# Kernel tuning notes

Hardware: AMD Instinct MI355X
Metric: run time of the kernel (lower is better)

The kernel has to match this reference:

```python
import jax, jax.numpy as jnp
import numpy as np

N = 50000   # nodes
E = 600000  # edges
D = 128     # in = hidden = out channels (must be equal per the cat/mean readout)
B = 4096    # number of lookup indices


def setup_inputs() -> dict:
    key = jax.random.key(0)
    ks = jax.random.split(key, 8)
    x = jax.random.normal(ks[0], (N, D), dtype=jnp.float32)
    edge_index = jax.random.randint(ks[1], (2, E), 0, N)
    edge_weight = jax.random.uniform(ks[2], (E,), dtype=jnp.float32)
    inputs_idx = jax.random.randint(ks[3], (B,), 0, N + 1)  # N is the appended zero row
    def lin_w(k, din, dout):
        return jax.random.normal(k, (din, dout), dtype=jnp.float32) / np.sqrt(din).astype(np.float32)
    W1 = lin_w(ks[4], D, D); b1 = jnp.zeros((D,), jnp.float32)
    W2 = lin_w(ks[5], D, D); b2 = jnp.zeros((D,), jnp.float32)
    W3 = lin_w(ks[6], D, D); b3 = jnp.zeros((D,), jnp.float32)
    return {"inputs_idx": inputs_idx, "x": x, "edge_index": edge_index,
            "edge_weight": edge_weight, "W1": W1, "b1": b1, "W2": W2,
            "b2": b2, "W3": W3, "b3": b3}


def gcn_conv(x, W, b, src, dst, w):
    # PyG GCNConv with add_self_loops=True (fill weight 1) and symmetric norm.
    deg = jnp.zeros((N,), x.dtype).at[dst].add(w) + 1.0  # self-loop contributes 1
    dinv = jax.lax.rsqrt(deg)
    norm = dinv[src] * w * dinv[dst]                      # [E]
    h = x @ W                                             # [N, D]
    agg = jax.ops.segment_sum(norm[:, None] * h[src], dst, num_segments=N)
    agg = agg + h * (dinv * dinv)[:, None]                # self-loop term: deg^-1 * h
    return agg + b


def lookup(x, inputs_idx):
    # append a zero row, then gather
    x_ = jnp.concatenate([x, jnp.zeros((1, x.shape[-1]), x.dtype)], axis=0)
    return x_[inputs_idx]  # [B, D]


def reference(inputs_idx, x, edge_index, edge_weight, W1, b1, W2, b2, W3, b3):
    src, dst = edge_index[0], edge_index[1]
    x1 = jax.nn.relu(gcn_conv(x, W1, b1, src, dst, edge_weight))
    x2 = jax.nn.relu(gcn_conv(x1, W2, b2, src, dst, edge_weight))
    x3 = jax.nn.relu(gcn_conv(x2, W3, b3, src, dst, edge_weight))
    e1 = lookup(x1, inputs_idx)
    e2 = lookup(x2, inputs_idx)
    e3 = lookup(x3, inputs_idx)
    # torch.cat([1,B,D]x3, dim=0).mean(0) == elementwise mean of the three
    return (e1 + e2 + e3) / 3.0
```

## Files before the change

### kernel.cpp

```cpp
#include <hip/hip_runtime.h>
#include <hip/hip_fp16.h>

#define D 128
#define STRIDE 48

typedef _Float16 f16x8 __attribute__((ext_vector_type(8)));
typedef float f32x4 __attribute__((ext_vector_type(4)));
struct h4 { __half2 a, b; };

__global__ __launch_bounds__(256) void zero_kernel(int* __restrict__ p, int n) {
  int i = blockIdx.x * 256 + threadIdx.x;
  if (i < n) p[i] = 0;
}

__global__ __launch_bounds__(256) void build_kernel(
    const int* __restrict__ ei, const float* __restrict__ ew,
    int* __restrict__ cnt, int2* __restrict__ pairs, int E) {
  int e = blockIdx.x * 256 + threadIdx.x;
  if (e >= E) return;
  int s = ei[e], d = ei[E + e];
  int rank = atomicAdd(&cnt[d], 1);
  if (rank < STRIDE) pairs[(size_t)d * STRIDE + rank] = make_int2(s, __float_as_int(ew[e]));
}

__global__ __launch_bounds__(256) void deg_dinv_kernel(
    int* __restrict__ cnt, const int2* __restrict__ pairs,
    float* __restrict__ dinv, int N) {
  int n = blockIdx.x * 4 + (threadIdx.x >> 6);
  int lane = threadIdx.x & 63;
  if (n >= N) return;
  int c = cnt[n];
  c = c < STRIDE ? c : STRIDE;
  float v = (lane < c) ? __int_as_float(pairs[(size_t)n * STRIDE + lane].y) : 0.f;
#pragma unroll
  for (int o = 32; o > 0; o >>= 1) v += __shfl_xor(v, o, 64);
  if (lane == 0) {
    dinv[n] = rsqrtf(v + 1.0f);
    cnt[n] = c;
  }
}

__global__ __launch_bounds__(256) void norm_kernel(
    const int* __restrict__ cnt, const float* __restrict__ dinv,
    int2* __restrict__ pairs, int N) {
  int n = blockIdx.x * 4 + (threadIdx.x >> 6);
  int lane = threadIdx.x & 63;
  if (n >= N) return;
  int c = cnt[n];
  float di = dinv[n];
  if (lane < c) {
    int2 p = pairs[(size_t)n * STRIDE + lane];
    p.y = __float_as_int(dinv[p.x] * __int_as_float(p.y) * di);
    pairs[(size_t)n * STRIDE + lane] = p;
  }
}

__global__ __launch_bounds__(256) void tohalf_kernel(
    const float* __restrict__ in, __half* __restrict__ out, int n4) {
  int t = blockIdx.x * 256 + threadIdx.x;
  if (t >= n4) return;
  float4 v = ((const float4*)in)[t];
  h4 o = {__floats2half2_rn(v.x, v.y), __floats2half2_rn(v.z, v.w)};
  ((h4*)out)[t] = o;
}

__global__ __launch_bounds__(256) void wtrans_kernel(
    const float* __restrict__ W1, const float* __restrict__ W2,
    const float* __restrict__ W3, __half* __restrict__ WT1,
    __half* __restrict__ WT2, __half* __restrict__ WT3) {
  int t = blockIdx.x * 256 + threadIdx.x;
  if (t >= 3 * D * D) return;
  int m = t >> 14;
  int i = t & (D * D - 1);
  int k = i >> 7, n = i & 127;
  const float* W = (m == 0) ? W1 : (m == 1) ? W2 : W3;
  __half* WT = (m == 0) ? WT1 : (m == 1) ? WT2 : WT3;
  WT[n * D + k] = __float2half(W[k * D + n]);
}

__global__ __launch_bounds__(256) void agg_kernel(
    const __half* __restrict__ x16, const float* __restrict__ dinv,
    const int* __restrict__ cnt, const int2* __restrict__ pairs,
    __half* __restrict__ agg16, int N) {
  int gw = (blockIdx.x * 256 + threadIdx.x) >> 6;
  int lane = threadIdx.x & 63;
  if (gw >= N) return;
  const __half2* xs = (const __half2*)x16;
  float di = dinv[gw];
  int c = cnt[gw];
  const int2* pr = pairs + (size_t)gw * STRIDE;
  float2 acc = __half22float2(xs[(size_t)gw * 64 + lane]);
  acc.x *= di * di;
  acc.y *= di * di;
  int e = 0;
  for (; e + 4 <= c; e += 4) {
    int2 p0 = pr[e], p1 = pr[e + 1], p2 = pr[e + 2], p3 = pr[e + 3];
    float n0 = __int_as_float(p0.y), n1 = __int_as_float(p1.y);
    float n2 = __int_as_float(p2.y), n3 = __int_as_float(p3.y);
    float2 v0 = __half22float2(xs[(size_t)p0.x * 64 + lane]);
    float2 v1 = __half22float2(xs[(size_t)p1.x * 64 + lane]);
    float2 v2 = __half22float2(xs[(size_t)p2.x * 64 + lane]);
    float2 v3 = __half22float2(xs[(size_t)p3.x * 64 + lane]);
    acc.x += n0 * v0.x + n1 * v1.x + n2 * v2.x + n3 * v3.x;
    acc.y += n0 * v0.y + n1 * v1.y + n2 * v2.y + n3 * v3.y;
  }
  for (; e < c; e++) {
    int2 p0 = pr[e];
    float n0 = __int_as_float(p0.y);
    float2 v0 = __half22float2(xs[(size_t)p0.x * 64 + lane]);
    acc.x += n0 * v0.x;
    acc.y += n0 * v0.y;
  }
  ((__half2*)agg16)[(size_t)gw * 64 + lane] = __floats2half2_rn(acc.x, acc.y);
}

__global__ __launch_bounds__(256) void agg_idx_kernel(
    const __half* __restrict__ x16, const float* __restrict__ dinv,
    const int* __restrict__ cnt, const int2* __restrict__ pairs,
    const int* __restrict__ idx, __half* __restrict__ aggI, int B, int N) {
  int gw = (blockIdx.x * 256 + threadIdx.x) >> 6;
  int lane = threadIdx.x & 63;
  if (gw >= B) return;
  const __half2* xs = (const __half2*)x16;
  float2 acc = make_float2(0.f, 0.f);
  int node = idx[gw];
  if ((unsigned)node < (unsigned)N) {
    float di = dinv[node];
    int c = cnt[node];
    const int2* pr = pairs + (size_t)node * STRIDE;
    acc = __half22float2(xs[(size_t)node * 64 + lane]);
    acc.x *= di * di;
    acc.y *= di * di;
    int e = 0;
    for (; e + 4 <= c; e += 4) {
      int2 p0 = pr[e], p1 = pr[e + 1], p2 = pr[e + 2], p3 = pr[e + 3];
      float n0 = __int_as_float(p0.y), n1 = __int_as_float(p1.y);
      float n2 = __int_as_float(p2.y), n3 = __int_as_float(p3.y);
      float2 v0 = __half22float2(xs[(size_t)p0.x * 64 + lane]);
      float2 v1 = __half22float2(xs[(size_t)p1.x * 64 + lane]);
      float2 v2 = __half22float2(xs[(size_t)p2.x * 64 + lane]);
      float2 v3 = __half22float2(xs[(size_t)p3.x * 64 + lane]);
      acc.x += n0 * v0.x + n1 * v1.x + n2 * v2.x + n3 * v3.x;
      acc.y += n0 * v0.y + n1 * v1.y + n2 * v2.y + n3 * v3.y;
    }
    for (; e < c; e++) {
      int2 p0 = pr[e];
      float n0 = __int_as_float(p0.y);
      float2 v0 = __half22float2(xs[(size_t)p0.x * 64 + lane]);
      acc.x += n0 * v0.x;
      acc.y += n0 * v0.y;
    }
  }
  ((__half2*)aggI)[(size_t)gw * 64 + lane] = __floats2half2_rn(acc.x, acc.y);
}

__global__ __launch_bounds__(256) void gemm16(
    const __half* __restrict__ A16, const __half* __restrict__ WT,
    const float* __restrict__ bias, __half* __restrict__ out16, int n) {
  __shared__ __half Bs[D * D];
  const int tid = threadIdx.x;
  const int wid = tid >> 6;
  const int lane = tid & 63;
  const int l15 = lane & 15;
  const int lk = lane >> 4;
  const int rbase = blockIdx.x * 64 + wid * 16;

  f16x8 a[4];
  {
    int r = rbase + l15;
    bool ok = (r < n);
    const __half* arow = A16 + (size_t)r * D + lk * 8;
#pragma unroll
    for (int kk = 0; kk < 4; kk++) {
      f16x8 z = {0, 0, 0, 0, 0, 0, 0, 0};
      a[kk] = ok ? *(const f16x8*)(arow + kk * 32) : z;
    }
  }
  {
    const int4* src = (const int4*)WT;
#pragma unroll
    for (int i = 0; i < 8; i++) {
      int slot = tid + i * 256;
      int byte = slot << 4;
      int row = byte >> 8;
      int4 v = src[slot];
      *(int4*)((char*)Bs + (byte ^ ((row & 7) << 4))) = v;
    }
  }
  __syncthreads();

  f32x4 c[8];
#pragma unroll
  for (int nf = 0; nf < 8; nf++) c[nf] = (f32x4){0.f, 0.f, 0.f, 0.f};

#pragma unroll
  for (int kk = 0; kk < 4; kk++) {
#pragma unroll
    for (int nf = 0; nf < 8; nf++) {
      int byte = ((nf * 16 + l15) << 8) + (kk << 6) + (lk << 4);
      byte ^= (l15 & 7) << 4;
      f16x8 b = *(const f16x8*)((const char*)Bs + byte);
      c[nf] = __builtin_amdgcn_mfma_f32_16x16x32_f16(a[kk], b, c[nf], 0, 0, 0);
    }
  }

#pragma unroll
  for (int nf = 0; nf < 8; nf++) {
    float bv = bias[nf * 16 + l15];
    int r0 = rbase + lk * 4;
#pragma unroll
    for (int rg = 0; rg < 4; rg++) {
      int r = r0 + rg;
      if (r < n) {
        float v = fmaxf(c[nf][rg] + bv, 0.f);
        out16[(size_t)r * D + nf * 16 + l15] = __float2half(v);
      }
    }
  }
}

__global__ __launch_bounds__(256) void lookup_kernel(
    const __half* __restrict__ xl, const int* __restrict__ idx,
    float* __restrict__ out, int B, int N, int add) {
  int t = blockIdx.x * 256 + threadIdx.x;
  if (t >= B * 16) return;
  int b = t >> 4, c8 = t & 15;
  int id = idx[b];
  float4 o0 = make_float4(0.f, 0.f, 0.f, 0.f);
  float4 o1 = make_float4(0.f, 0.f, 0.f, 0.f);
  if ((unsigned)id < (unsigned)N) {
    int4 raw = *(const int4*)(xl + (size_t)id * D + c8 * 8);
    const __half2* h = (const __half2*)&raw;
    float2 f0 = __half22float2(h[0]);
    float2 f1 = __half22float2(h[1]);
    float2 f2 = __half22float2(h[2]);
    float2 f3 = __half22float2(h[3]);
    o0 = make_float4(f0.x, f0.y, f1.x, f1.y);
    o1 = make_float4(f2.x, f2.y, f3.x, f3.y);
  }
  const float s = 1.0f / 3.0f;
  float* op = out + (size_t)b * D + c8 * 8;
  if (add) {
    float4 p0 = *(float4*)op, p1 = *(float4*)(op + 4);
    p0.x += o0.x * s; p0.y += o0.y * s; p0.z += o0.z * s; p0.w += o0.w * s;
    p1.x += o1.x * s; p1.y += o1.y * s; p1.z += o1.z * s; p1.w += o1.w * s;
    *(float4*)op = p0; *(float4*)(op + 4) = p1;
  } else {
    float4 p0 = make_float4(o0.x * s, o0.y * s, o0.z * s, o0.w * s);
    float4 p1 = make_float4(o1.x * s, o1.y * s, o1.z * s, o1.w * s);
    *(float4*)op = p0; *(float4*)(op + 4) = p1;
  }
}

__global__ __launch_bounds__(256) void lookup_direct_kernel(
    const __half* __restrict__ oC, const int* __restrict__ idx,
    float* __restrict__ out, int B, int N) {
  int t = blockIdx.x * 256 + threadIdx.x;
  if (t >= B * 16) return;
  int b = t >> 4, c8 = t & 15;
  if ((unsigned)idx[b] >= (unsigned)N) return;
  int4 raw = *(const int4*)(oC + (size_t)b * D + c8 * 8);
  const __half2* h = (const __half2*)&raw;
  float2 f0 = __half22float2(h[0]);
  float2 f1 = __half22float2(h[1]);
  float2 f2 = __half22float2(h[2]);
  float2 f3 = __half22float2(h[3]);
  const float s = 1.0f / 3.0f;
  float* op = out + (size_t)b * D + c8 * 8;
  float4 p0 = *(float4*)op, p1 = *(float4*)(op + 4);
  p0.x += f0.x * s; p0.y += f0.y * s; p0.z += f1.x * s; p0.w += f1.y * s;
  p1.x += f2.x * s; p1.y += f2.y * s; p1.z += f3.x * s; p1.w += f3.y * s;
  *(float4*)op = p0; *(float4*)(op + 4) = p1;
}


extern "C" void kernel_launch(void* const* d_in, const int* in_sizes, int n_in,
                              void* d_out, int out_size, void* d_ws, size_t ws_size,
                              hipStream_t stream) {
  const int*   inputs_idx  = (const int*)d_in[0];
  const float* x           = (const float*)d_in[1];
  const int*   edge_index  = (const int*)d_in[2];
  const float* edge_weight = (const float*)d_in[3];
  const float* W1 = (const float*)d_in[4];
  const float* b1 = (const float*)d_in[5];
  const float* W2 = (const float*)d_in[6];
  const float* b2 = (const float*)d_in[7];
  const float* W3 = (const float*)d_in[8];
  const float* b3 = (const float*)d_in[9];
  float* out = (float*)d_out;

  const int B = in_sizes[0];
  const int N = in_sizes[1] / D;
  const int E = in_sizes[3];
  (void)n_in; (void)out_size; (void)ws_size;

  char* p = (char*)d_ws;
  size_t off = 0;
  auto alloc = [&](size_t bytes) -> void* {
    void* r = p + off;
    off += (bytes + 255) & ~(size_t)255;
    return r;
  };
  int*    cnt   = (int*)alloc((size_t)N * 4);
  float*  dinv  = (float*)alloc((size_t)N * 4);
  int2*   pairs = (int2*)alloc((size_t)N * STRIDE * 8);
  __half* x16   = (__half*)alloc((size_t)N * D * 2);
  __half* aggT  = (__half*)alloc((size_t)N * D * 2);
  __half* oA    = (__half*)alloc((size_t)N * D * 2);
  __half* oB    = (__half*)alloc((size_t)N * D * 2);
  __half* WT1   = (__half*)alloc((size_t)D * D * 2);
  __half* WT2   = (__half*)alloc((size_t)D * D * 2);
  __half* WT3   = (__half*)alloc((size_t)D * D * 2);

  int eb = (E + 255) / 256;
  int wb = (N + 3) / 4;
  zero_kernel<<<(N + 255) / 256, 256, 0, stream>>>(cnt, N);
  build_kernel<<<eb, 256, 0, stream>>>(edge_index, edge_weight, cnt, pairs, E);
  deg_dinv_kernel<<<wb, 256, 0, stream>>>(cnt, pairs, dinv, N);
  norm_kernel<<<wb, 256, 0, stream>>>(cnt, dinv, pairs, N);
  tohalf_kernel<<<(N * 32 + 255) / 256, 256, 0, stream>>>(x, x16, N * 32);
  wtrans_kernel<<<(3 * D * D + 255) / 256, 256, 0, stream>>>(W1, W2, W3, WT1, WT2, WT3);

  int ab = (N + 3) / 4;
  int gb = (N + 63) / 64;
  int lb = (B * 16 + 255) / 256;

  agg_kernel<<<ab, 256, 0, stream>>>(x16, dinv, cnt, pairs, aggT, N);
  gemm16<<<gb, 256, 0, stream>>>(aggT, WT1, b1, oA, N);
  lookup_kernel<<<lb, 256, 0, stream>>>(oA, inputs_idx, out, B, N, 0);
  agg_kernel<<<ab, 256, 0, stream>>>(oA, dinv, cnt, pairs, aggT, N);
  gemm16<<<gb, 256, 0, stream>>>(aggT, WT2, b2, oB, N);
  lookup_kernel<<<lb, 256, 0, stream>>>(oB, inputs_idx, out, B, N, 1);
  int ib = (B + 3) / 4;
  int gb3 = (B + 63) / 64;
  agg_idx_kernel<<<ib, 256, 0, stream>>>(oB, dinv, cnt, pairs, inputs_idx, aggT, B, N);
  gemm16<<<gb3, 256, 0, stream>>>(aggT, WT3, b3, oA, B);
  lookup_direct_kernel<<<lb, 256, 0, stream>>>(oA, inputs_idx, out, B, N);
}
```

Measured before the change: 176.9 us.

## Fuse three lookups into one combine kernel and double GEMM rows per wave

```diff
diff --git a/kernel.cpp b/kernel.cpp
--- a/kernel.cpp
+++ b/kernel.cpp
@@ -163,17 +163,18 @@
   const int lane = tid & 63;
   const int l15 = lane & 15;
   const int lk = lane >> 4;
-  const int rbase = blockIdx.x * 64 + wid * 16;
-
-  f16x8 a[4];
-  {
-    int r = rbase + l15;
+  const int rbase = blockIdx.x * 128 + wid * 32;
+
+  f16x8 a[2][4];
+#pragma unroll
+  for (int m = 0; m < 2; m++) {
+    int r = rbase + m * 16 + l15;
     bool ok = (r < n);
     const __half* arow = A16 + (size_t)r * D + lk * 8;
 #pragma unroll
     for (int kk = 0; kk < 4; kk++) {
       f16x8 z = {0, 0, 0, 0, 0, 0, 0, 0};
-      a[kk] = ok ? *(const f16x8*)(arow + kk * 32) : z;
+      a[m][kk] = ok ? *(const f16x8*)(arow + kk * 32) : z;
     }
   }
   {
@@ -189,9 +190,11 @@
   }
   __syncthreads();
 
-  f32x4 c[8];
-#pragma unroll
-  for (int nf = 0; nf < 8; nf++) c[nf] = (f32x4){0.f, 0.f, 0.f, 0.f};
+  f32x4 c[2][8];
+#pragma unroll
+  for (int m = 0; m < 2; m++)
+#pragma unroll
+    for (int nf = 0; nf < 8; nf++) c[m][nf] = (f32x4){0.f, 0.f, 0.f, 0.f};
 
 #pragma unroll
   for (int kk = 0; kk < 4; kk++) {
@@ -200,77 +203,59 @@
       int byte = ((nf * 16 + l15) << 8) + (kk << 6) + (lk << 4);
       byte ^= (l15 & 7) << 4;
       f16x8 b = *(const f16x8*)((const char*)Bs + byte);
-      c[nf] = __builtin_amdgcn_mfma_f32_16x16x32_f16(a[kk], b, c[nf], 0, 0, 0);
+      c[0][nf] = __builtin_amdgcn_mfma_f32_16x16x32_f16(a[0][kk], b, c[0][nf], 0, 0, 0);
+      c[1][nf] = __builtin_amdgcn_mfma_f32_16x16x32_f16(a[1][kk], b, c[1][nf], 0, 0, 0);
     }
   }
 
 #pragma unroll
   for (int nf = 0; nf < 8; nf++) {
     float bv = bias[nf * 16 + l15];
-    int r0 = rbase + lk * 4;
-#pragma unroll
-    for (int rg = 0; rg < 4; rg++) {
-      int r = r0 + rg;
-      if (r < n) {
-        float v = fmaxf(c[nf][rg] + bv, 0.f);
-        out16[(size_t)r * D + nf * 16 + l15] = __float2half(v);
+#pragma unroll
+    for (int m = 0; m < 2; m++) {
+      int r0 = rbase + m * 16 + lk * 4;
+#pragma unroll
+      for (int rg = 0; rg < 4; rg++) {
+        int r = r0 + rg;
+        if (r < n) {
+          float v = fmaxf(c[m][nf][rg] + bv, 0.f);
+          out16[(size_t)r * D + nf * 16 + l15] = __float2half(v);
+        }
       }
     }
   }
 }
 
-__global__ __launch_bounds__(256) void lookup_kernel(
-    const __half* __restrict__ xl, const int* __restrict__ idx,
-    float* __restrict__ out, int B, int N, int add) {
-  int t = blockIdx.x * 256 + threadIdx.x;
-  if (t >= B * 16) return;
-  int b = t >> 4, c8 = t & 15;
-  int id = idx[b];
-  float4 o0 = make_float4(0.f, 0.f, 0.f, 0.f);
-  float4 o1 = make_float4(0.f, 0.f, 0.f, 0.f);
-  if ((unsigned)id < (unsigned)N) {
-    int4 raw = *(const int4*)(xl + (size_t)id * D + c8 * 8);
-    const __half2* h = (const __half2*)&raw;
-    float2 f0 = __half22float2(h[0]);
-    float2 f1 = __half22float2(h[1]);
-    float2 f2 = __half22float2(h[2]);
-    float2 f3 = __half22float2(h[3]);
-    o0 = make_float4(f0.x, f0.y, f1.x, f1.y);
-    o1 = make_float4(f2.x, f2.y, f3.x, f3.y);
-  }
-  const float s = 1.0f / 3.0f;
-  float* op = out + (size_t)b * D + c8 * 8;
-  if (add) {
-    float4 p0 = *(float4*)op, p1 = *(float4*)(op + 4);
-    p0.x += o0.x * s; p0.y += o0.y * s; p0.z += o0.z * s; p0.w += o0.w * s;
-    p1.x += o1.x * s; p1.y += o1.y * s; p1.z += o1.z * s; p1.w += o1.w * s;
-    *(float4*)op = p0; *(float4*)(op + 4) = p1;
-  } else {
-    float4 p0 = make_float4(o0.x * s, o0.y * s, o0.z * s, o0.w * s);
-    float4 p1 = make_float4(o1.x * s, o1.y * s, o1.z * s, o1.w * s);
-    *(float4*)op = p0; *(float4*)(op + 4) = p1;
-  }
-}
-
-__global__ __launch_bounds__(256) void lookup_direct_kernel(
+__global__ __launch_bounds__(256) void combine_kernel(
+    const __half* __restrict__ oA, const __half* __restrict__ oB,
     const __half* __restrict__ oC, const int* __restrict__ idx,
     float* __restrict__ out, int B, int N) {
   int t = blockIdx.x * 256 + threadIdx.x;
   if (t >= B * 16) return;
   int b = t >> 4, c8 = t & 15;
-  if ((unsigned)idx[b] >= (unsigned)N) return;
-  int4 raw = *(const int4*)(oC + (size_t)b * D + c8 * 8);
-  const __half2* h = (const __half2*)&raw;
-  float2 f0 = __half22float2(h[0]);
-  float2 f1 = __half22float2(h[1]);
-  float2 f2 = __half22float2(h[2]);
-  float2 f3 = __half22float2(h[3]);
-  const float s = 1.0f / 3.0f;
+  int id = idx[b];
+  float4 p0 = make_float4(0.f, 0.f, 0.f, 0.f);
+  float4 p1 = make_float4(0.f, 0.f, 0.f, 0.f);
+  if ((unsigned)id < (unsigned)N) {
+    int4 r1 = *(const int4*)(oA + (size_t)id * D + c8 * 8);
+    int4 r2 = *(const int4*)(oB + (size_t)id * D + c8 * 8);
+    int4 r3 = *(const int4*)(oC + (size_t)b * D + c8 * 8);
+    const __half2 *h1 = (const __half2*)&r1, *h2 = (const __half2*)&r2,
+                  *h3 = (const __half2*)&r3;
+#pragma unroll
+    for (int j = 0; j < 4; j++) {
+      float2 f1 = __half22float2(h1[j]);
+      float2 f2 = __half22float2(h2[j]);
+      float2 f3 = __half22float2(h3[j]);
+      float sx = (f1.x + f2.x + f3.x) * (1.0f / 3.0f);
+      float sy = (f1.y + f2.y + f3.y) * (1.0f / 3.0f);
+      if (j < 2) { ((float*)&p0)[j * 2] = sx; ((float*)&p0)[j * 2 + 1] = sy; }
+      else       { ((float*)&p1)[(j - 2) * 2] = sx; ((float*)&p1)[(j - 2) * 2 + 1] = sy; }
+    }
+  }
   float* op = out + (size_t)b * D + c8 * 8;
-  float4 p0 = *(float4*)op, p1 = *(float4*)(op + 4);
-  p0.x += f0.x * s; p0.y += f0.y * s; p0.z += f1.x * s; p0.w += f1.y * s;
-  p1.x += f2.x * s; p1.y += f2.y * s; p1.z += f3.x * s; p1.w += f3.y * s;
-  *(float4*)op = p0; *(float4*)(op + 4) = p1;
+  *(float4*)op = p0;
+  *(float4*)(op + 4) = p1;
 }
 
 
@@ -308,6 +293,7 @@
   __half* aggT  = (__half*)alloc((size_t)N * D * 2);
   __half* oA    = (__half*)alloc((size_t)N * D * 2);
   __half* oB    = (__half*)alloc((size_t)N * D * 2);
+  __half* oC    = (__half*)alloc((size_t)B * D * 2);
   __half* WT1   = (__half*)alloc((size_t)D * D * 2);
   __half* WT2   = (__half*)alloc((size_t)D * D * 2);
   __half* WT3   = (__half*)alloc((size_t)D * D * 2);
@@ -322,18 +308,16 @@
   wtrans_kernel<<<(3 * D * D + 255) / 256, 256, 0, stream>>>(W1, W2, W3, WT1, WT2, WT3);
 
   int ab = (N + 3) / 4;
-  int gb = (N + 63) / 64;
+  int gb = (N + 127) / 128;
   int lb = (B * 16 + 255) / 256;
 
   agg_kernel<<<ab, 256, 0, stream>>>(x16, dinv, cnt, pairs, aggT, N);
   gemm16<<<gb, 256, 0, stream>>>(aggT, WT1, b1, oA, N);
-  lookup_kernel<<<lb, 256, 0, stream>>>(oA, inputs_idx, out, B, N, 0);
   agg_kernel<<<ab, 256, 0, stream>>>(oA, dinv, cnt, pairs, aggT, N);
   gemm16<<<gb, 256, 0, stream>>>(aggT, WT2, b2, oB, N);
-  lookup_kernel<<<lb, 256, 0, stream>>>(oB, inputs_idx, out, B, N, 1);
   int ib = (B + 3) / 4;
-  int gb3 = (B + 63) / 64;
+  int gb3 = (B + 127) / 128;
   agg_idx_kernel<<<ib, 256, 0, stream>>>(oB, dinv, cnt, pairs, inputs_idx, aggT, B, N);
-  gemm16<<<gb3, 256, 0, stream>>>(aggT, WT3, b3, oA, B);
-  lookup_direct_kernel<<<lb, 256, 0, stream>>>(oA, inputs_idx, out, B, N);
-}
+  gemm16<<<gb3, 256, 0, stream>>>(aggT, WT3, b3, oC, B);
+  combine_kernel<<<lb, 256, 0, stream>>>(oA, oB, oC, inputs_idx, out, B, N);
+}
```

New measurement: 186.7 us. 5.5% more time.
